# Kernel optimization log

Measured on AMD Instinct MI355X. Metric: run time of the kernel, lower is better.

Reference implementation:

```python
import jax, jax.numpy as jnp
import numpy as np

NUM_HEADS = 16
HEAD_DIM = 128  # 2048 / 16


def setup_inputs() -> dict:
    key = jax.random.key(0)
    ks = jax.random.split(key, 5)
    B, S, D = 2, 2048, 2048
    scale = 1.0 / np.sqrt(D)
    return {
        "x": jax.random.normal(ks[0], (B, S, D), dtype=jnp.float32),
        "Wq": jax.random.normal(ks[1], (D, D), dtype=jnp.float32) * scale,
        "Wk": jax.random.normal(ks[2], (D, D), dtype=jnp.float32) * scale,
        "Wv": jax.random.normal(ks[3], (D, D), dtype=jnp.float32) * scale,
        "Wo": jax.random.normal(ks[4], (D, D), dtype=jnp.float32) * scale,
    }


def reference(x, Wq, Wk, Wv, Wo):
    B, S, D = x.shape
    H, Hd = NUM_HEADS, HEAD_DIM
    # nn.Linear(bias=False): y = x @ W.T
    q = (x @ Wq.T).reshape(B, S, H, Hd).transpose(0, 2, 1, 3)  # [B,H,S,Hd]
    k = (x @ Wk.T).reshape(B, S, H, Hd).transpose(0, 2, 1, 3)
    v = (x @ Wv.T).reshape(B, S, H, Hd).transpose(0, 2, 1, 3)
    scores = jnp.einsum("bhqd,bhkd->bhqk", q, k) / jnp.sqrt(jnp.float32(Hd))
    attn = jax.nn.softmax(scores, axis=-1)  # dropout p=0 (eval) -> identity
    out = jnp.einsum("bhqk,bhkd->bhqd", attn, v)  # [B,H,S,Hd]
    out = out.transpose(0, 2, 1, 3).reshape(B, S, D)
    out = out @ Wo.T
    return out
```

## Files before the change

### kernel.cpp

```cpp
#include <hip/hip_runtime.h>
#include <math.h>
#include <stdint.h>


#define DDIM 2048
#define SEQ  2048
#define NH   16
#define HD   128

typedef __attribute__((ext_vector_type(4))) float f32x4;
typedef __attribute__((ext_vector_type(16))) float f32x16;
typedef __attribute__((ext_vector_type(8))) __bf16 bf16x8;
typedef __attribute__((ext_vector_type(4))) unsigned int u32x4;
typedef __attribute__((ext_vector_type(2))) unsigned int u32x2;

#define MFMA_B16(a, b, c) __builtin_amdgcn_mfma_f32_16x16x32_bf16((a), (b), (c), 0, 0, 0)
#define MFMA32(a, b, c) __builtin_amdgcn_mfma_f32_32x32x16_bf16((a), (b), (c), 0, 0, 0)

__device__ __forceinline__ void async16(const void* g, void* l) {
  __builtin_amdgcn_global_load_lds(
      (const __attribute__((address_space(1))) unsigned int*)g,
      (__attribute__((address_space(3))) unsigned int*)l, 16, 0, 0);
}

__device__ __forceinline__ unsigned short f2bf(float f) {
  unsigned u = __builtin_bit_cast(unsigned, f);
  u += 0x7fffu + ((u >> 16) & 1u);
  return (unsigned short)(u >> 16);
}

__device__ __forceinline__ bf16x8 ldfrag(const unsigned short* p) {
  return __builtin_bit_cast(bf16x8, *(const u32x4*)p);
}

__device__ __forceinline__ void cvt_body(const float* __restrict__ s,
                                         unsigned short* __restrict__ d, int i) {
  const f32x4* sp = (const f32x4*)s;
  f32x4 a = sp[2 * i], b = sp[2 * i + 1];
  u32x4 o;
  o.x = ((unsigned)f2bf(a.y) << 16) | f2bf(a.x);
  o.y = ((unsigned)f2bf(a.w) << 16) | f2bf(a.z);
  o.z = ((unsigned)f2bf(b.y) << 16) | f2bf(b.x);
  o.w = ((unsigned)f2bf(b.w) << 16) | f2bf(b.z);
  ((u32x4*)d)[i] = o;
}

__global__ __launch_bounds__(256) void cvt_bf16_kernel(const float* __restrict__ s,
                                                       unsigned short* __restrict__ d) {
  cvt_body(s, d, blockIdx.x * 256 + threadIdx.x);
}

__global__ __launch_bounds__(256) void cvt_all_kernel(const float* __restrict__ x,
                                                      const float* __restrict__ wq,
                                                      const float* __restrict__ wk,
                                                      const float* __restrict__ wv,
                                                      const float* __restrict__ wo,
                                                      unsigned short* __restrict__ xb,
                                                      unsigned short* __restrict__ wqkv,
                                                      unsigned short* __restrict__ wob) {
  const int b = blockIdx.x;
  if (b < 4096) {
    cvt_body(x, xb, b * 256 + threadIdx.x);
  } else if (b < 10240) {
    const int wi = (b - 4096) >> 11, lb = (b - 4096) & 2047;
    const float* s = (wi == 0) ? wq : (wi == 1) ? wk : wv;
    cvt_body(s, wqkv + (size_t)wi * 4194304u, lb * 256 + threadIdx.x);
  } else {
    cvt_body(wo, wob, (b - 10240) * 256 + threadIdx.x);
  }
}

__global__ __launch_bounds__(256) void gemm_qkv(const unsigned short* __restrict__ A,
                                                const unsigned short* __restrict__ B,
                                                unsigned short* __restrict__ Oqk,
                                                unsigned short* __restrict__ Ovt,
                                                float alpha_q) {
  __shared__ unsigned short As[128 * 64];
  __shared__ unsigned short Bs[128 * 64];
  const int tid = threadIdx.x;
  const int lane = tid & 63, w = tid >> 6;
  const int l32 = lane & 31, half = lane >> 5;
  const int wm = (w >> 1) * 64, wn = (w & 1) * 64;
  const int bm = blockIdx.y * 128, bn = blockIdx.x * 128;

  f32x16 acc[2][2];
#pragma unroll
  for (int i = 0; i < 2; ++i)
#pragma unroll
    for (int j = 0; j < 2; ++j)
#pragma unroll
      for (int e = 0; e < 16; ++e) acc[i][j][e] = 0.f;

  const unsigned short* pa[4];
  const unsigned short* pbb[4];
  {
#pragma unroll
    for (int j = 0; j < 4; ++j) {
      const int row = j * 32 + (tid >> 3);
      const int cg = (tid & 7) ^ (row & 7) ^ ((row >> 3) & 7);
      pa[j] = A + (size_t)(bm + row) * DDIM + cg * 8;
      pbb[j] = B + (size_t)(bn + row) * DDIM + cg * 8;
    }
  }

  const int fr = (l32 & 7) ^ (l32 >> 3);

  for (int kt = 0; kt < 32; ++kt) {
    __syncthreads();
#pragma unroll
    for (int j = 0; j < 4; ++j) {
      async16(pa[j], &As[(j * 256 + tid) * 8]);
      pa[j] += 64;
      async16(pbb[j], &Bs[(j * 256 + tid) * 8]);
      pbb[j] += 64;
    }
    __syncthreads();
#pragma unroll
    for (int ks = 0; ks < 4; ++ks) {
      const int ph = ks * 2 + half;
      const int sl0 = (ph ^ fr) * 8;
      const int sl1 = (ph ^ fr ^ 4) * 8;
      bf16x8 af0 = ldfrag(&As[(wm + l32) * 64 + sl0]);
      bf16x8 af1 = ldfrag(&As[(wm + 32 + l32) * 64 + sl1]);
      bf16x8 bf0 = ldfrag(&Bs[(wn + l32) * 64 + sl0]);
      bf16x8 bf1 = ldfrag(&Bs[(wn + 32 + l32) * 64 + sl1]);
      acc[0][0] = MFMA32(af0, bf0, acc[0][0]);
      acc[0][1] = MFMA32(af0, bf1, acc[0][1]);
      acc[1][0] = MFMA32(af1, bf0, acc[1][0]);
      acc[1][1] = MFMA32(af1, bf1, acc[1][1]);
    }
  }

  const int seg = bn >> 11;
  const int bnl = bn & 2047;
  const float alpha = (seg == 0) ? alpha_q : 1.0f;
#pragma unroll
  for (int i = 0; i < 2; ++i) {
#pragma unroll
    for (int j = 0; j < 2; ++j) {
#pragma unroll
      for (int rg = 0; rg < 4; ++rg) {
        const int m0 = bm + wm + i * 32 + rg * 8 + half * 4;
        const float v0 = acc[i][j][rg * 4 + 0] * alpha;
        const float v1 = acc[i][j][rg * 4 + 1] * alpha;
        const float v2 = acc[i][j][rg * 4 + 2] * alpha;
        const float v3 = acc[i][j][rg * 4 + 3] * alpha;
        const int n = bnl + wn + j * 32 + l32;
        if (seg < 2) {
          unsigned short* O = Oqk + (size_t)seg * (4096u * 2048u);
          O[(size_t)(m0 + 0) * DDIM + n] = f2bf(v0);
          O[(size_t)(m0 + 1) * DDIM + n] = f2bf(v1);
          O[(size_t)(m0 + 2) * DDIM + n] = f2bf(v2);
          O[(size_t)(m0 + 3) * DDIM + n] = f2bf(v3);
        } else {
          const int bb = m0 >> 11, s0 = m0 & 2047;
          const int hh = n >> 7, dd = n & 127;
          u32x2 st;
          st.x = ((unsigned)f2bf(v1) << 16) | f2bf(v0);
          st.y = ((unsigned)f2bf(v3) << 16) | f2bf(v2);
          *(u32x2*)&Ovt[((size_t)((bb * NH + hh) * HD + dd)) * SEQ + s0] = st;
        }
      }
    }
  }
}

__global__ __launch_bounds__(256) void gemm_o64(const unsigned short* __restrict__ A,
                                                const unsigned short* __restrict__ B,
                                                float* __restrict__ Cf) {
  __shared__ unsigned short As[128 * 64];
  __shared__ unsigned short Bs[64 * 64];
  const int tid = threadIdx.x;
  const int lane = tid & 63, w = tid >> 6;
  const int l32 = lane & 31, half = lane >> 5;
  const int wm = (w >> 1) * 64, wn = (w & 1) * 32;
  const int bm = blockIdx.y * 128, bn = blockIdx.x * 64;

  f32x16 acc[2];
#pragma unroll
  for (int i = 0; i < 2; ++i)
#pragma unroll
    for (int e = 0; e < 16; ++e) acc[i][e] = 0.f;

  const unsigned short* pa[4];
  const unsigned short* pbb[2];
  {
#pragma unroll
    for (int j = 0; j < 4; ++j) {
      const int row = j * 32 + (tid >> 3);
      const int cg = (tid & 7) ^ (row & 7) ^ ((row >> 3) & 7);
      pa[j] = A + (size_t)(bm + row) * DDIM + cg * 8;
      if (j < 2) pbb[j] = B + (size_t)(bn + row) * DDIM + cg * 8;
    }
  }

  const int fr = (l32 & 7) ^ (l32 >> 3);
  const int fb = fr ^ ((wn >> 3) & 4);

  for (int kt = 0; kt < 32; ++kt) {
    __syncthreads();
#pragma unroll
    for (int j = 0; j < 4; ++j) {
      async16(pa[j], &As[(j * 256 + tid) * 8]);
      pa[j] += 64;
      if (j < 2) {
        async16(pbb[j], &Bs[(j * 256 + tid) * 8]);
        pbb[j] += 64;
      }
    }
    __syncthreads();
#pragma unroll
    for (int ks = 0; ks < 4; ++ks) {
      const int ph = ks * 2 + half;
      bf16x8 af0 = ldfrag(&As[(wm + l32) * 64 + (ph ^ fr) * 8]);
      bf16x8 af1 = ldfrag(&As[(wm + 32 + l32) * 64 + (ph ^ fr ^ 4) * 8]);
      bf16x8 bf0 = ldfrag(&Bs[(wn + l32) * 64 + (ph ^ fb) * 8]);
      acc[0] = MFMA32(af0, bf0, acc[0]);
      acc[1] = MFMA32(af1, bf0, acc[1]);
    }
  }

#pragma unroll
  for (int i = 0; i < 2; ++i) {
#pragma unroll
    for (int rg = 0; rg < 4; ++rg) {
      const int m0 = bm + wm + i * 32 + rg * 8 + half * 4;
      const int n = bn + wn + l32;
      Cf[(size_t)(m0 + 0) * DDIM + n] = acc[i][rg * 4 + 0];
      Cf[(size_t)(m0 + 1) * DDIM + n] = acc[i][rg * 4 + 1];
      Cf[(size_t)(m0 + 2) * DDIM + n] = acc[i][rg * 4 + 2];
      Cf[(size_t)(m0 + 3) * DDIM + n] = acc[i][rg * 4 + 3];
    }
  }
}

__global__ __launch_bounds__(512) void attn_kernel(const unsigned short* __restrict__ qb,
                                                   const unsigned short* __restrict__ kb,
                                                   const unsigned short* __restrict__ vtb,
                                                   unsigned short* __restrict__ ab) {
  __shared__ unsigned short Ks[2][64 * 128];
  __shared__ unsigned short Vts[2][128 * 64];
  __shared__ unsigned short Pw[8 * 16 * 40];
  const int tid = threadIdx.x;
  const int w = tid >> 6, lane = tid & 63;
  const int quad = lane >> 4, l16 = lane & 15;
  const int qt = blockIdx.x, bh = blockIdx.y;
  const int b = bh >> 4, h = bh & 15;
  const int qrow = qt * 128 + w * 16 + l16;

  const unsigned short* qp = qb + ((size_t)(b * SEQ + qrow)) * DDIM + h * HD;
  bf16x8 qf[4];
#pragma unroll
  for (int ks = 0; ks < 4; ++ks) qf[ks] = ldfrag(qp + ks * 32 + quad * 8);

  f32x4 ot[8];
#pragma unroll
  for (int i = 0; i < 8; i++) ot[i] = f32x4{0.f, 0.f, 0.f, 0.f};
  float sumacc = 0.f;

  const unsigned short* kp[2];
  const unsigned short* vp[2];
  {
    const size_t kbase = ((size_t)(b * SEQ)) * DDIM + h * HD;
    const size_t vbase = ((size_t)((b * NH + h) * HD)) * SEQ;
#pragma unroll
    for (int j = 0; j < 2; ++j) {
      const int key = j * 32 + (tid >> 4), cgk = (tid & 15) ^ (key & 15);
      kp[j] = kb + kbase + (size_t)key * DDIM + cgk * 8;
      const int dd = j * 64 + (tid >> 3), cgv = (tid & 7) ^ (dd & 7);
      vp[j] = vtb + vbase + (size_t)dd * SEQ + cgv * 8;
    }
  }
  unsigned short* pw = &Pw[w * 640];

#pragma unroll
  for (int j = 0; j < 2; ++j) {
    async16(kp[j], &Ks[0][(j * 512 + tid) * 8]);
    async16(vp[j], &Vts[0][(j * 512 + tid) * 8]);
  }
  __syncthreads();

  for (int kt = 0; kt < SEQ / 64; ++kt) {
    const int cur = kt & 1, nxt = cur ^ 1;
    {
      const int t1 = (kt + 1) & 31;
      const size_t koff = (size_t)(t1 * 64) * DDIM;
      const int voff = t1 * 64;
#pragma unroll
      for (int j = 0; j < 2; ++j) {
        async16(kp[j] + koff, &Ks[nxt][(j * 512 + tid) * 8]);
        async16(vp[j] + voff, &Vts[nxt][(j * 512 + tid) * 8]);
      }
    }
    f32x4 s[4];
#pragma unroll
    for (int t = 0; t < 4; ++t) s[t] = f32x4{0.f, 0.f, 0.f, 0.f};
#pragma unroll
    for (int ks = 0; ks < 4; ++ks) {
      const int sl = ((ks * 4 + quad) ^ l16) * 8;
#pragma unroll
      for (int t = 0; t < 4; ++t) {
        bf16x8 a = ldfrag(&Ks[cur][(t * 16 + l16) * 128 + sl]);
        s[t] = MFMA_B16(a, qf[ks], s[t]);
      }
    }
    f32x4 p[4];
#pragma unroll
    for (int t = 0; t < 4; ++t) {
      p[t].x = __builtin_amdgcn_exp2f(s[t].x);
      p[t].y = __builtin_amdgcn_exp2f(s[t].y);
      p[t].z = __builtin_amdgcn_exp2f(s[t].z);
      p[t].w = __builtin_amdgcn_exp2f(s[t].w);
      sumacc += (p[t].x + p[t].y) + (p[t].z + p[t].w);
    }
    bf16x8 pb0, pb1;
    {
      u32x2 w0, w1;
      w0.x = ((unsigned)f2bf(p[0].y) << 16) | f2bf(p[0].x);
      w0.y = ((unsigned)f2bf(p[0].w) << 16) | f2bf(p[0].z);
      w1.x = ((unsigned)f2bf(p[1].y) << 16) | f2bf(p[1].x);
      w1.y = ((unsigned)f2bf(p[1].w) << 16) | f2bf(p[1].z);
      *(u32x2*)&pw[l16 * 40 + quad * 4] = w0;
      *(u32x2*)&pw[l16 * 40 + 16 + quad * 4] = w1;
      asm volatile("s_waitcnt lgkmcnt(0)" ::: "memory");
      pb0 = ldfrag(&pw[l16 * 40 + quad * 8]);
      w0.x = ((unsigned)f2bf(p[2].y) << 16) | f2bf(p[2].x);
      w0.y = ((unsigned)f2bf(p[2].w) << 16) | f2bf(p[2].z);
      w1.x = ((unsigned)f2bf(p[3].y) << 16) | f2bf(p[3].x);
      w1.y = ((unsigned)f2bf(p[3].w) << 16) | f2bf(p[3].z);
      *(u32x2*)&pw[l16 * 40 + quad * 4] = w0;
      *(u32x2*)&pw[l16 * 40 + 16 + quad * 4] = w1;
      asm volatile("s_waitcnt lgkmcnt(0)" ::: "memory");
      pb1 = ldfrag(&pw[l16 * 40 + quad * 8]);
    }
#pragma unroll
    for (int mt = 0; mt < 8; ++mt) {
      bf16x8 vf0 = ldfrag(&Vts[cur][(mt * 16 + l16) * 64 + (quad ^ (l16 & 7)) * 8]);
      ot[mt] = MFMA_B16(vf0, pb0, ot[mt]);
      bf16x8 vf1 = ldfrag(&Vts[cur][(mt * 16 + l16) * 64 + ((4 + quad) ^ (l16 & 7)) * 8]);
      ot[mt] = MFMA_B16(vf1, pb1, ot[mt]);
    }
    __syncthreads();
  }
  float total = sumacc;
  total += __shfl_xor(total, 16);
  total += __shfl_xor(total, 32);
  const float inv = 1.0f / total;
  unsigned short* op = ab + ((size_t)(b * SEQ + qrow)) * DDIM + h * HD;
#pragma unroll
  for (int mt = 0; mt < 8; ++mt) {
    f32x4 v = ot[mt] * inv;
    u32x2 st;
    st.x = ((unsigned)f2bf(v.y) << 16) | f2bf(v.x);
    st.y = ((unsigned)f2bf(v.w) << 16) | f2bf(v.z);
    *(u32x2*)&op[mt * 16 + quad * 4] = st;
  }
}

extern "C" void kernel_launch(void* const* d_in, const int* in_sizes, int n_in,
                              void* d_out, int out_size, void* d_ws, size_t ws_size,
                              hipStream_t stream) {
  (void)in_sizes; (void)n_in; (void)out_size;
  const float* x = (const float*)d_in[0];
  const float* Wq = (const float*)d_in[1];
  const float* Wk = (const float*)d_in[2];
  const float* Wv = (const float*)d_in[3];
  const float* Wo = (const float*)d_in[4];

  char* ws = (char*)d_ws;
  unsigned short* xb = (unsigned short*)(ws);
  unsigned short* wqkv = (unsigned short*)(ws + 16777216);
  unsigned short* qb = (unsigned short*)(ws + 41943040);
  unsigned short* kb = (unsigned short*)(ws + 58720256);
  unsigned short* vtb = (unsigned short*)(ws + 75497472);
  const bool big = ws_size >= 100663296ull;
  unsigned short* wob = big ? (unsigned short*)(ws + 92274688) : wqkv;

  const float alpha_q = 1.44269504088896341f / sqrtf(128.0f);

  if (big) {
    cvt_all_kernel<<<dim3(12288), 256, 0, stream>>>(x, Wq, Wk, Wv, Wo, xb, wqkv, wob);
    gemm_qkv<<<dim3(48, 32), 256, 0, stream>>>(xb, wqkv, qb, vtb, alpha_q);
  } else {
    cvt_all_kernel<<<dim3(10240), 256, 0, stream>>>(x, Wq, Wk, Wv, Wo, xb, wqkv, wob);
    gemm_qkv<<<dim3(48, 32), 256, 0, stream>>>(xb, wqkv, qb, vtb, alpha_q);
    cvt_bf16_kernel<<<dim3(2048), 256, 0, stream>>>(Wo, wob);
  }

  attn_kernel<<<dim3(16, 32), 512, 0, stream>>>(qb, kb, vtb, xb);

  gemm_o64<<<dim3(32, 32), 256, 0, stream>>>(xb, wob, (float*)d_out);
}
```

Before: 369.8 us.

## Double-buffer LDS in QKV GEMM and interleave fragment reads with MFMAs

The QKV projection GEMM now uses two LDS buffers. The next K tile is fetched asynchronously while MFMAs run on the current one, and fragment loads are software-pipelined one k-step ahead using explicit lgkmcnt waits, sched barriers and setprio around the MFMA groups. This hides global-to-LDS latency and the two full syncthreads per iteration that the old loop paid. In exchange it doubles LDS use, which may lower occupancy, and it relies on hand-placed waitcnt and barrier ordering. The last iteration prefetches a wrapped-around tile that is never used.

Measured after the change: 393.2 us. 6.3% more time.

```diff
diff --git a/kernel.cpp b/kernel.cpp
--- a/kernel.cpp
+++ b/kernel.cpp
@@ -70,13 +70,48 @@
   }
 }
 
+#define STGQ_A(BUF, CB)                                            \
+  {                                                                \
+    _Pragma("unroll") for (int j = 0; j < 4; ++j)                  \
+        async16(pa[j] + (CB), &As[BUF][(j * 256 + tid) * 8]);      \
+  }
+#define STGQ_B(BUF, CB)                                            \
+  {                                                                \
+    _Pragma("unroll") for (int j = 0; j < 4; ++j)                  \
+        async16(pbb[j] + (CB), &Bs[BUF][(j * 256 + tid) * 8]);     \
+  }
+
+#define READ4(CUR, KS, F)                                            \
+  {                                                                  \
+    const int ph_ = (KS) * 2 + half;                                 \
+    const int sl0_ = (ph_ ^ fr) * 8, sl1_ = (ph_ ^ fr ^ 4) * 8;      \
+    F[0] = ldfrag(&As[CUR][(wm + l32) * 64 + sl0_]);                 \
+    F[1] = ldfrag(&As[CUR][(wm + 32 + l32) * 64 + sl1_]);            \
+    F[2] = ldfrag(&Bs[CUR][(wn + l32) * 64 + sl0_]);                 \
+    F[3] = ldfrag(&Bs[CUR][(wn + 32 + l32) * 64 + sl1_]);            \
+  }
+
+#define LGKM4                                            \
+  do {                                                   \
+    asm volatile("s_waitcnt lgkmcnt(4)" ::: "memory");   \
+    __builtin_amdgcn_sched_barrier(0);                   \
+  } while (0)
+
+#define MFMA4(F)                                         \
+  __builtin_amdgcn_s_setprio(1);                         \
+  acc[0][0] = MFMA32(F[0], F[2], acc[0][0]);             \
+  acc[0][1] = MFMA32(F[0], F[3], acc[0][1]);             \
+  acc[1][0] = MFMA32(F[1], F[2], acc[1][0]);             \
+  acc[1][1] = MFMA32(F[1], F[3], acc[1][1]);             \
+  __builtin_amdgcn_s_setprio(0);
+
 __global__ __launch_bounds__(256) void gemm_qkv(const unsigned short* __restrict__ A,
                                                 const unsigned short* __restrict__ B,
                                                 unsigned short* __restrict__ Oqk,
                                                 unsigned short* __restrict__ Ovt,
                                                 float alpha_q) {
-  __shared__ unsigned short As[128 * 64];
-  __shared__ unsigned short Bs[128 * 64];
+  __shared__ unsigned short As[2][128 * 64];
+  __shared__ unsigned short Bs[2][128 * 64];
   const int tid = threadIdx.x;
   const int lane = tid & 63, w = tid >> 6;
   const int l32 = lane & 31, half = lane >> 5;
@@ -105,31 +140,37 @@
 
   const int fr = (l32 & 7) ^ (l32 >> 3);
 
+  bf16x8 fX[4], fY[4];
+
+  STGQ_A(0, 0);
+  STGQ_B(0, 0);
+  asm volatile("s_waitcnt vmcnt(0)" ::: "memory");
+  __builtin_amdgcn_s_barrier();
+  READ4(0, 0, fX);
+
+#pragma unroll 1
   for (int kt = 0; kt < 32; ++kt) {
-    __syncthreads();
-#pragma unroll
-    for (int j = 0; j < 4; ++j) {
-      async16(pa[j], &As[(j * 256 + tid) * 8]);
-      pa[j] += 64;
-      async16(pbb[j], &Bs[(j * 256 + tid) * 8]);
-      pbb[j] += 64;
-    }
-    __syncthreads();
-#pragma unroll
-    for (int ks = 0; ks < 4; ++ks) {
-      const int ph = ks * 2 + half;
-      const int sl0 = (ph ^ fr) * 8;
-      const int sl1 = (ph ^ fr ^ 4) * 8;
-      bf16x8 af0 = ldfrag(&As[(wm + l32) * 64 + sl0]);
-      bf16x8 af1 = ldfrag(&As[(wm + 32 + l32) * 64 + sl1]);
-      bf16x8 bf0 = ldfrag(&Bs[(wn + l32) * 64 + sl0]);
-      bf16x8 bf1 = ldfrag(&Bs[(wn + 32 + l32) * 64 + sl1]);
-      acc[0][0] = MFMA32(af0, bf0, acc[0][0]);
-      acc[0][1] = MFMA32(af0, bf1, acc[0][1]);
-      acc[1][0] = MFMA32(af1, bf0, acc[1][0]);
-      acc[1][1] = MFMA32(af1, bf1, acc[1][1]);
-    }
-  }
+    const int cur = kt & 1, nxt = cur ^ 1;
+    const int cb = ((kt + 1) & 31) * 64;
+    READ4(cur, 1, fY);
+    STGQ_A(nxt, cb);
+    LGKM4;
+    MFMA4(fX);
+    READ4(cur, 2, fX);
+    STGQ_B(nxt, cb);
+    LGKM4;
+    MFMA4(fY);
+    READ4(cur, 3, fY);
+    LGKM4;
+    MFMA4(fX);
+    asm volatile("s_waitcnt vmcnt(0)" ::: "memory");
+    __builtin_amdgcn_s_barrier();
+    READ4(nxt, 0, fX);
+    LGKM4;
+    MFMA4(fY);
+    __builtin_amdgcn_s_barrier();
+  }
+  asm volatile("s_waitcnt vmcnt(0) lgkmcnt(0)" ::: "memory");
 
   const int seg = bn >> 11;
   const int bnl = bn & 2047;
```
